# Kernel optimization log

Measured on AMD Instinct MI355X. Metric: run time of the kernel, lower is better.

The kernel has to match this reference:

```python
import jax, jax.numpy as jnp
import numpy as np


def setup_inputs() -> dict:
    key = jax.random.key(0)
    ks = jax.random.split(key, 7)
    b, d, n, l = 2, 1024, 16, 2048
    u = jax.random.normal(ks[0], (b, d, l), dtype=jnp.float32)
    delta = jax.random.normal(ks[1], (b, d, l), dtype=jnp.float32)
    # A negative for stable decay, as in Mamba (A = -exp(A_log))
    A = -jax.random.uniform(ks[2], (d, n), dtype=jnp.float32, minval=0.5, maxval=4.0)
    B = jax.random.normal(ks[3], (b, n, l), dtype=jnp.float32)
    C = jax.random.normal(ks[4], (b, n, l), dtype=jnp.float32)
    D = jax.random.normal(ks[5], (d,), dtype=jnp.float32)
    z = jax.random.normal(ks[6], (b, d, l), dtype=jnp.float32)
    return {"u": u, "delta": delta, "A": A, "B": B, "C": C, "D": D, "z": z,
            "delta_softplus": 1}


def _selective_scan(u, delta, A, B, C, D, z):
    # u, delta, z: (b, d, l); A: (d, n); B, C: (b, n, l); D: (d,)
    # Recurrence per (b, d, n):  h_t = exp(delta_t * A) * h_{t-1} + delta_t * B_t * u_t
    deltaA = jnp.exp(delta[:, :, None, :] * A[None, :, :, None])          # (b, d, n, l)
    deltaBu = (delta * u)[:, :, None, :] * B[:, None, :, :]               # (b, d, n, l)

    def combine(c1, c2):
        a1, x1 = c1
        a2, x2 = c2
        return a1 * a2, a2 * x1 + x2

    _, h = jax.lax.associative_scan(combine, (deltaA, deltaBu), axis=-1)  # h: (b, d, n, l)
    y = jnp.einsum('bnl,bdnl->bdl', C, h)
    y = y + u * D[None, :, None]
    y = y * jax.nn.silu(z)
    return y.astype(u.dtype)


def reference(u, delta, A, B, C, D, z, delta_softplus):
    # delta_softplus is asserted True in the original module
    delta = jax.nn.softplus(delta)
    return _selective_scan(u, delta, A, B, C, D, z)
```

## Files before the change

### kernel.cpp

```cpp
#include <hip/hip_runtime.h>
#include <cstdint>

constexpr int kD = 1024;
constexpr int kN = 16;
constexpr int kL = 2048;
constexpr int BLOCK = 512;
constexpr int T  = kL / BLOCK;
constexpr int NW = BLOCK / 64;
constexpr int NQ = 4;
constexpr int NP = kN / NQ;
constexpr float LOG2E = 1.44269504088896340736f;

__device__ __forceinline__ float fast_exp2(float x) { return __builtin_amdgcn_exp2f(x); }
__device__ __forceinline__ float fast_exp(float x)  { return __builtin_amdgcn_exp2f(x * LOG2E); }
__device__ __forceinline__ float softplus_f(float x) {
  return (x > 20.0f) ? x : __logf(1.0f + fast_exp(x));
}

template<int CTRL, int RM>
__device__ __forceinline__ float dppf(float old_, float src) {
  union U { float f; int i; };
  U o, s, r; o.f = old_; s.f = src;
  r.i = __builtin_amdgcn_update_dpp(o.i, s.i, CTRL, RM, 0xF, false);
  return r.f;
}

__device__ __forceinline__ float readlane_f(float v, int l) {
  union U { float f; int i; };
  U a, r; a.f = v;
  r.i = __builtin_amdgcn_readlane(a.i, l);
  return r.f;
}

#define SCAN_FM(X, A, CTRL) \
  "v_fmac_f32_dpp " X ", " X ", " A " " CTRL "\n\t" \
  "v_mul_f32_dpp "  A ", " A ", " A " " CTRL "\n\t"
#define SCAN_STEP(CTRL) \
  SCAN_FM("%0","%4",CTRL) SCAN_FM("%1","%5",CTRL) \
  SCAN_FM("%2","%6",CTRL) SCAN_FM("%3","%7",CTRL)

__global__ __launch_bounds__(BLOCK)
void selscan_kernel(const float* __restrict__ u,  const float* __restrict__ dl,
                    const float* __restrict__ A,  const float* __restrict__ Bm,
                    const float* __restrict__ Cm, const float* __restrict__ Dv,
                    const float* __restrict__ zm, float* __restrict__ out)
{
  const int row  = blockIdx.x;
  const int b    = row >> 10;
  const int d    = row & (kD - 1);
  const int tid  = threadIdx.x;
  const int lane = tid & 63;
  const int wid  = tid >> 6;

  const size_t roff = (size_t)row * kL;
  const float4* u4 = reinterpret_cast<const float4*>(u  + roff);
  const float4* d4 = reinterpret_cast<const float4*>(dl + roff);

  float spl[T], du[T];
  {
    float4 a0 = u4[tid];
    float4 b0 = d4[tid];
    float uv[T] = {a0.x, a0.y, a0.z, a0.w};
    float dv[T] = {b0.x, b0.y, b0.z, b0.w};
    #pragma unroll
    for (int i = 0; i < T; ++i) {
      float s = softplus_f(dv[i]);
      du[i]  = s * uv[i];
      spl[i] = s * LOG2E;
    }
  }

  float y[T];
  #pragma unroll
  for (int i = 0; i < T; ++i) y[i] = 0.0f;

  __shared__ float2 sAX[NP][NW][NQ];

  #pragma unroll 1
  for (int q = 0; q < NP; ++q) {
    float Aq[NQ];
    {
      const float4 av = *reinterpret_cast<const float4*>(A + (size_t)d * kN + q * NQ);
      Aq[0] = av.x; Aq[1] = av.y; Aq[2] = av.z; Aq[3] = av.w;
    }
    const float4* B4 = reinterpret_cast<const float4*>(Bm + ((size_t)b * kN + q * NQ) * kL);
    const float4* C4 = reinterpret_cast<const float4*>(Cm + ((size_t)b * kN + q * NQ) * kL);

    float cp[NQ][T];
    float cA[NQ], cX[NQ];
    #pragma unroll
    for (int n = 0; n < NQ; ++n) {
      float4 b0 = B4[n * (kL / 4) + tid];
      float4 c0 = C4[n * (kL / 4) + tid];
      float Bv[T] = {b0.x, b0.y, b0.z, b0.w};
      float Cv[T] = {c0.x, c0.y, c0.z, c0.w};
      float h = 0.0f, p = 1.0f;
      #pragma unroll
      for (int i = 0; i < T; ++i) {
        float a = fast_exp2(spl[i] * Aq[n]);
        h = a * h + du[i] * Bv[i];
        p *= a;
        y[i] += Cv[i] * h;
        cp[n][i] = Cv[i] * p;
      }
      cA[n] = p; cX[n] = h;
    }

    {
      float x0=cX[0], x1=cX[1], x2=cX[2], x3=cX[3];
      float a0=cA[0], a1=cA[1], a2=cA[2], a3=cA[3];
      asm("s_nop 1\n\t"
          SCAN_STEP("row_shr:1 row_mask:0xf bank_mask:0xf")
          SCAN_STEP("row_shr:2 row_mask:0xf bank_mask:0xf")
          SCAN_STEP("row_shr:4 row_mask:0xf bank_mask:0xf")
          SCAN_STEP("row_shr:8 row_mask:0xf bank_mask:0xf")
          SCAN_STEP("row_bcast:15 row_mask:0xa bank_mask:0xf")
          SCAN_STEP("row_bcast:31 row_mask:0xc bank_mask:0xf")
          : "+v"(x0), "+v"(x1), "+v"(x2), "+v"(x3),
            "+v"(a0), "+v"(a1), "+v"(a2), "+v"(a3));
      cX[0]=x0; cX[1]=x1; cX[2]=x2; cX[3]=x3;
      cA[0]=a0; cA[1]=a1; cA[2]=a2; cA[3]=a3;
    }

    if (lane == 63) {
      #pragma unroll
      for (int n = 0; n < NQ; ++n) sAX[q][wid][n] = make_float2(cA[n], cX[n]);
    }
    __syncthreads();

    float ex = 0.0f;
    {
      const int n = lane & (NQ - 1);
      float2 s[NW - 1];
      #pragma unroll
      for (int w2 = 0; w2 < NW - 1; ++w2) s[w2] = sAX[q][w2][n];
      #pragma unroll
      for (int w2 = 0; w2 < NW - 1; ++w2) {
        float aa = (w2 < wid) ? s[w2].x : 1.0f;
        float xx = (w2 < wid) ? s[w2].y : 0.0f;
        ex = aa * ex + xx;
      }
    }

    #pragma unroll
    for (int n = 0; n < NQ; ++n) {
      float al = dppf<0x138,0xF>(1.0f, cA[n]);
      float xl = dppf<0x138,0xF>(0.0f, cX[n]);
      float exn = readlane_f(ex, n);
      float h0 = al * exn + xl;
      #pragma unroll
      for (int i = 0; i < T; ++i) y[i] += cp[n][i] * h0;
    }
  }

  const float Dd = Dv[d];
  const float4* z4 = reinterpret_cast<const float4*>(zm + roff);
  float4 z0 = z4[tid];
  float4 a0 = u4[tid];
  float zv[T] = {z0.x, z0.y, z0.z, z0.w};
  float uv[T] = {a0.x, a0.y, a0.z, a0.w};
  float ov[T];
  #pragma unroll
  for (int i = 0; i < T; ++i) {
    float yy  = y[i] + uv[i] * Dd;
    float sig = 1.0f / (1.0f + fast_exp(-zv[i]));
    ov[i] = yy * zv[i] * sig;
  }
  reinterpret_cast<float4*>(out + roff)[tid] = make_float4(ov[0], ov[1], ov[2], ov[3]);
}

extern "C" void kernel_launch(void* const* d_in, const int* in_sizes, int n_in,
                              void* d_out, int out_size, void* d_ws, size_t ws_size,
                              hipStream_t stream)
{
  const float* u  = (const float*)d_in[0];
  const float* dl = (const float*)d_in[1];
  const float* A  = (const float*)d_in[2];
  const float* Bm = (const float*)d_in[3];
  const float* Cm = (const float*)d_in[4];
  const float* Dv = (const float*)d_in[5];
  const float* zm = (const float*)d_in[6];
  float* out = (float*)d_out;
  const int rows = in_sizes[0] / kL;
  selscan_kernel<<<rows, BLOCK, 0, stream>>>(u, dl, A, Bm, Cm, Dv, zm, out);
}
```

Before: 126.5 us.

## Prefetch next B/C chunk into LDS via async global_load_lds during scan

Half of the B and C rows for each state group are now staged into shared memory with async global-to-LDS loads. The loads for the next group are issued before the cross-wave barrier, so they overlap the wave scan and carry phase. The remaining rows are still loaded directly, and the explicit waitcnt plus s_barrier replaces __syncthreads. This adds 32KB of LDS per block, which may lower occupancy, and the hand-coded waitcnt encodings risk being wrong or too conservative.

```diff
diff --git a/kernel.cpp b/kernel.cpp
--- a/kernel.cpp
+++ b/kernel.cpp
@@ -11,10 +11,19 @@
 constexpr int NP = kN / NQ;
 constexpr float LOG2E = 1.44269504088896340736f;
 
+constexpr unsigned WAIT_LGKM0 = 0xC07F;
+constexpr unsigned WAIT_VM0   = 0x0F70;
+
 __device__ __forceinline__ float fast_exp2(float x) { return __builtin_amdgcn_exp2f(x); }
 __device__ __forceinline__ float fast_exp(float x)  { return __builtin_amdgcn_exp2f(x * LOG2E); }
 __device__ __forceinline__ float softplus_f(float x) {
   return (x > 20.0f) ? x : __logf(1.0f + fast_exp(x));
+}
+
+__device__ __forceinline__ void stage16(const float* g, float* l) {
+  __builtin_amdgcn_global_load_lds(
+      (const __attribute__((address_space(1))) void*)g,
+      (__attribute__((address_space(3))) void*)l, 16, 0, 0);
 }
 
 template<int CTRL, int RM>
@@ -38,6 +47,13 @@
 #define SCAN_STEP(CTRL) \
   SCAN_FM("%0","%4",CTRL) SCAN_FM("%1","%5",CTRL) \
   SCAN_FM("%2","%6",CTRL) SCAN_FM("%3","%7",CTRL)
+
+#define SSTEP(i, Bc, Cc) {                         \
+    float a_ = fast_exp2(spl[i] * Arn);            \
+    h = fmaf(a_, h, du[i] * (Bc));                 \
+    p *= a_;                                       \
+    y[i] = fmaf((Cc), h, y[i]);                    \
+    cp[n][i] = (Cc) * p; }
 
 __global__ __launch_bounds__(BLOCK)
 void selscan_kernel(const float* __restrict__ u,  const float* __restrict__ dl,
@@ -55,13 +71,23 @@
   const size_t roff = (size_t)row * kL;
   const float4* u4 = reinterpret_cast<const float4*>(u  + roff);
   const float4* d4 = reinterpret_cast<const float4*>(dl + roff);
+  const float4* B4all = reinterpret_cast<const float4*>(Bm + (size_t)b * kN * kL);
+  const float4* C4all = reinterpret_cast<const float4*>(Cm + (size_t)b * kN * kL);
+
+  __shared__ float4 stg[2][2][BLOCK];
+  __shared__ float2 sAX[NP][NW][NQ];
+
+  float4 a0 = u4[tid];
+  float4 b0_ = d4[tid];
+  stage16((const float*)&B4all[0 * (kL/4) + tid], (float*)&stg[0][0][tid]);
+  stage16((const float*)&B4all[1 * (kL/4) + tid], (float*)&stg[0][1][tid]);
+  stage16((const float*)&C4all[0 * (kL/4) + tid], (float*)&stg[1][0][tid]);
+  stage16((const float*)&C4all[1 * (kL/4) + tid], (float*)&stg[1][1][tid]);
 
   float spl[T], du[T];
   {
-    float4 a0 = u4[tid];
-    float4 b0 = d4[tid];
     float uv[T] = {a0.x, a0.y, a0.z, a0.w};
-    float dv[T] = {b0.x, b0.y, b0.z, b0.w};
+    float dv[T] = {b0_.x, b0_.y, b0_.z, b0_.w};
     #pragma unroll
     for (int i = 0; i < T; ++i) {
       float s = softplus_f(dv[i]);
@@ -74,8 +100,6 @@
   #pragma unroll
   for (int i = 0; i < T; ++i) y[i] = 0.0f;
 
-  __shared__ float2 sAX[NP][NW][NQ];
-
   #pragma unroll 1
   for (int q = 0; q < NP; ++q) {
     float Aq[NQ];
@@ -83,32 +107,41 @@
       const float4 av = *reinterpret_cast<const float4*>(A + (size_t)d * kN + q * NQ);
       Aq[0] = av.x; Aq[1] = av.y; Aq[2] = av.z; Aq[3] = av.w;
     }
-    const float4* B4 = reinterpret_cast<const float4*>(Bm + ((size_t)b * kN + q * NQ) * kL);
-    const float4* C4 = reinterpret_cast<const float4*>(Cm + ((size_t)b * kN + q * NQ) * kL);
+    const float4* Bq = B4all + (size_t)(q * NQ) * (kL/4);
+    const float4* Cq = C4all + (size_t)(q * NQ) * (kL/4);
+
+    __builtin_amdgcn_s_waitcnt(WAIT_VM0);
+    __builtin_amdgcn_sched_barrier(0);
+
+    float4 b2 = Bq[2 * (kL/4) + tid];
+    float4 c2 = Cq[2 * (kL/4) + tid];
+    float4 b3 = Bq[3 * (kL/4) + tid];
+    float4 c3 = Cq[3 * (kL/4) + tid];
+    float4 b0 = stg[0][0][tid];
+    float4 b1 = stg[0][1][tid];
+    float4 c0 = stg[1][0][tid];
+    float4 c1 = stg[1][1][tid];
 
     float cp[NQ][T];
     float cA[NQ], cX[NQ];
-    #pragma unroll
-    for (int n = 0; n < NQ; ++n) {
-      float4 b0 = B4[n * (kL / 4) + tid];
-      float4 c0 = C4[n * (kL / 4) + tid];
-      float Bv[T] = {b0.x, b0.y, b0.z, b0.w};
-      float Cv[T] = {c0.x, c0.y, c0.z, c0.w};
-      float h = 0.0f, p = 1.0f;
-      #pragma unroll
-      for (int i = 0; i < T; ++i) {
-        float a = fast_exp2(spl[i] * Aq[n]);
-        h = a * h + du[i] * Bv[i];
-        p *= a;
-        y[i] += Cv[i] * h;
-        cp[n][i] = Cv[i] * p;
-      }
-      cA[n] = p; cX[n] = h;
+    {
+      { const int n = 0; const float Arn = Aq[0]; float h = 0.f, p = 1.f;
+        SSTEP(0, b0.x, c0.x) SSTEP(1, b0.y, c0.y) SSTEP(2, b0.z, c0.z) SSTEP(3, b0.w, c0.w)
+        cA[n] = p; cX[n] = h; }
+      { const int n = 1; const float Arn = Aq[1]; float h = 0.f, p = 1.f;
+        SSTEP(0, b1.x, c1.x) SSTEP(1, b1.y, c1.y) SSTEP(2, b1.z, c1.z) SSTEP(3, b1.w, c1.w)
+        cA[n] = p; cX[n] = h; }
+      { const int n = 2; const float Arn = Aq[2]; float h = 0.f, p = 1.f;
+        SSTEP(0, b2.x, c2.x) SSTEP(1, b2.y, c2.y) SSTEP(2, b2.z, c2.z) SSTEP(3, b2.w, c2.w)
+        cA[n] = p; cX[n] = h; }
+      { const int n = 3; const float Arn = Aq[3]; float h = 0.f, p = 1.f;
+        SSTEP(0, b3.x, c3.x) SSTEP(1, b3.y, c3.y) SSTEP(2, b3.z, c3.z) SSTEP(3, b3.w, c3.w)
+        cA[n] = p; cX[n] = h; }
     }
 
     {
       float x0=cX[0], x1=cX[1], x2=cX[2], x3=cX[3];
-      float a0=cA[0], a1=cA[1], a2=cA[2], a3=cA[3];
+      float a0_=cA[0], a1_=cA[1], a2_=cA[2], a3_=cA[3];
       asm("s_nop 1\n\t"
           SCAN_STEP("row_shr:1 row_mask:0xf bank_mask:0xf")
           SCAN_STEP("row_shr:2 row_mask:0xf bank_mask:0xf")
@@ -117,16 +150,27 @@
           SCAN_STEP("row_bcast:15 row_mask:0xa bank_mask:0xf")
           SCAN_STEP("row_bcast:31 row_mask:0xc bank_mask:0xf")
           : "+v"(x0), "+v"(x1), "+v"(x2), "+v"(x3),
-            "+v"(a0), "+v"(a1), "+v"(a2), "+v"(a3));
+            "+v"(a0_), "+v"(a1_), "+v"(a2_), "+v"(a3_));
       cX[0]=x0; cX[1]=x1; cX[2]=x2; cX[3]=x3;
-      cA[0]=a0; cA[1]=a1; cA[2]=a2; cA[3]=a3;
+      cA[0]=a0_; cA[1]=a1_; cA[2]=a2_; cA[3]=a3_;
     }
 
     if (lane == 63) {
       #pragma unroll
       for (int n = 0; n < NQ; ++n) sAX[q][wid][n] = make_float2(cA[n], cX[n]);
     }
-    __syncthreads();
+
+    if (q < NP - 1) {
+      const float4* Bn = B4all + (size_t)((q + 1) * NQ) * (kL/4);
+      const float4* Cn = C4all + (size_t)((q + 1) * NQ) * (kL/4);
+      stage16((const float*)&Bn[0 * (kL/4) + tid], (float*)&stg[0][0][tid]);
+      stage16((const float*)&Bn[1 * (kL/4) + tid], (float*)&stg[0][1][tid]);
+      stage16((const float*)&Cn[0 * (kL/4) + tid], (float*)&stg[1][0][tid]);
+      stage16((const float*)&Cn[1 * (kL/4) + tid], (float*)&stg[1][1][tid]);
+    }
+
+    __builtin_amdgcn_s_waitcnt(WAIT_LGKM0);
+    __builtin_amdgcn_s_barrier();
 
     float ex = 0.0f;
     {
@@ -156,9 +200,9 @@
   const float Dd = Dv[d];
   const float4* z4 = reinterpret_cast<const float4*>(zm + roff);
   float4 z0 = z4[tid];
-  float4 a0 = u4[tid];
+  float4 ua = u4[tid];
   float zv[T] = {z0.x, z0.y, z0.z, z0.w};
-  float uv[T] = {a0.x, a0.y, a0.z, a0.w};
+  float uv[T] = {ua.x, ua.y, ua.z, ua.w};
   float ov[T];
   #pragma unroll
   for (int i = 0; i < T; ++i) {
```

Result: no change. 125.9 us (-0.5%).
